# Kernel tuning notes

Measured on AMD Instinct MI355X. Metric: run time of the kernel, lower is better.

## Reference

```python
import jax, jax.numpy as jnp
import numpy as np

B, N, D, E = 4, 4096, 1024, 64
EPS = 1e-9
THRESH = 0.2            # second_threshold_eval
CAP_FACTOR = 2.0        # capacity_factor_eval
MIN_EXPERT_CAPACITY = 4


def setup_inputs() -> dict:
    key = jax.random.key(0)
    k1, k2 = jax.random.split(key)
    x = jax.random.normal(k1, (B, N, D), dtype=jnp.float32)
    w_gating = jax.random.normal(k2, (D, E), dtype=jnp.float32)
    return {"x": x, "w_gating": w_gating}


def _cumsum_exclusive(t, axis):
    # exclusive cumsum along `axis` (equivalent to pad-then-cumsum-then-slice)
    return jnp.cumsum(t, axis=axis) - t


def _gating(x, w_gating):
    b, n, d = x.shape
    e = w_gating.shape[-1]
    dt = x.dtype

    gate_logits = jnp.einsum('bnd,de->bne', x, w_gating)   # [b,n,e]
    raw_gates = jax.nn.softmax(gate_logits, axis=-1)

    index_1 = jnp.argmax(raw_gates, axis=-1)               # [b,n]
    gate_1 = jnp.max(raw_gates, axis=-1)                   # [b,n]
    mask_1 = jax.nn.one_hot(index_1, e, dtype=dt)          # [b,n,e]
    density_1_proxy = raw_gates

    gates_without_top_1 = raw_gates * (1.0 - mask_1)
    index_2 = jnp.argmax(gates_without_top_1, axis=-1)
    gate_2 = jnp.max(gates_without_top_1, axis=-1)
    mask_2 = jax.nn.one_hot(index_2, e, dtype=dt)

    denom = gate_1 + gate_2 + EPS
    gate_1 = gate_1 / denom
    gate_2 = gate_2 / denom

    # load-balancing aux loss
    density_1 = jnp.mean(mask_1, axis=-2)                  # [b,e]
    density_proxy = jnp.mean(density_1_proxy, axis=-2)     # [b,e]
    loss = jnp.mean(density_proxy * density_1) * float(e * e)

    # second-expert policy: 'threshold'
    mask_2 = mask_2 * (gate_2 > THRESH).astype(dt)[..., None]

    expert_capacity = max(min(n, int(n * CAP_FACTOR / e)), MIN_EXPERT_CAPACITY)
    cap_f = float(expert_capacity)

    # capacity routing for top-1
    position_in_expert_1 = _cumsum_exclusive(mask_1, axis=-2) * mask_1
    mask_1 = mask_1 * (position_in_expert_1 < cap_f).astype(dt)
    mask_1_count = jnp.sum(mask_1, axis=-2, keepdims=True)  # [b,1,e]
    mask_1_flat = jnp.sum(mask_1, axis=-1)                  # [b,n]
    position_in_expert_1 = jnp.sum(position_in_expert_1, axis=-1)  # [b,n]
    gate_1 = gate_1 * mask_1_flat

    # capacity routing for top-2 (offset by top-1 counts)
    position_in_expert_2 = (_cumsum_exclusive(mask_2, axis=-2) + mask_1_count) * mask_2
    mask_2 = mask_2 * (position_in_expert_2 < cap_f).astype(dt)
    mask_2_flat = jnp.sum(mask_2, axis=-1)
    position_in_expert_2 = jnp.sum(position_in_expert_2, axis=-1)
    gate_2 = gate_2 * mask_2_flat

    # one_hot with out-of-range index -> all zeros, matching safe_one_hot's clipping
    oh_e1 = jax.nn.one_hot(index_1, e, dtype=dt)
    oh_e2 = jax.nn.one_hot(index_2, e, dtype=dt)
    oh_c1 = jax.nn.one_hot(position_in_expert_1.astype(jnp.int32), expert_capacity, dtype=dt)
    oh_c2 = jax.nn.one_hot(position_in_expert_2.astype(jnp.int32), expert_capacity, dtype=dt)

    combine_tensor = (
        (gate_1 * mask_1_flat)[..., None, None] * oh_e1[..., :, None] * oh_c1[..., None, :]
        + (gate_2 * mask_2_flat)[..., None, None] * oh_e2[..., :, None] * oh_c2[..., None, :]
    )  # [b,n,e,capacity]

    router_z_loss = jnp.mean(jnp.sum(jax.nn.logsumexp(gate_logits, axis=-1), axis=-1))
    return combine_tensor, loss, router_z_loss


def reference(x, w_gating):
    combine_tensor, loss, router_z_loss = _gating(x, w_gating)
    dispatch_tensor = (combine_tensor != 0).astype(combine_tensor.dtype)
    return dispatch_tensor, combine_tensor, loss, router_z_loss
```

## Files before the change

kernel.cpp:

```cpp
#include <hip/hip_runtime.h>


#define B_DIM 4
#define N_DIM 4096
#define D_DIM 1024
#define E_DIM 64
#define CAP   128
#define NTOK  (B_DIM * N_DIM)
#define TM    32
#define TK    64
#define GATE_BLOCKS 512
#define ZERO_BLOCKS 8192

#define WS_IDX1  0
#define WS_IDX2  65536
#define WS_G1    131072
#define WS_G2    196608
#define WS_DENS  262144
#define WS_ZSUM  263168

__global__ __launch_bounds__(256) void fused_gating_zero(
    const float* __restrict__ x, const float* __restrict__ w,
    int* __restrict__ idx1, int* __restrict__ idx2,
    float* __restrict__ g1o, float* __restrict__ g2o,
    float* __restrict__ dens, float* __restrict__ zsum,
    float* __restrict__ out, size_t half) {
  __shared__ __align__(16) char smem[(TM * 68 + TK * E_DIM) * 4];
  const int t = threadIdx.x;

  if (blockIdx.x >= GATE_BLOCKS) {
    const int zb = blockIdx.x - GATE_BLOCKS;
    float4* o4 = (float4*)out;
    const size_t base = (size_t)zb * (256 * 32) + t;
    const float4 z = make_float4(0.f, 0.f, 0.f, 0.f);
#pragma unroll
    for (int i = 0; i < 32; ++i) o4[base + (size_t)i * 256] = z;
    if (zb == 0 && t == 0) { out[2 * half] = 0.f; out[2 * half + 1] = 0.f; }
    return;
  }

  float (*As)[68]   = (float(*)[68])smem;
  float (*Bs)[E_DIM] = (float(*)[E_DIM])(smem + TM * 68 * 4);
  double (*Ld)[65]  = (double(*)[65])smem;

  const int tokBase = blockIdx.x * TM;
  const int e4 = t & 15;
  const int tokg = t >> 4;
  const int tok0 = 2 * tokg, e0 = 4 * e4;

  double acc[2][4] = {};

  for (int k0 = 0; k0 < D_DIM; k0 += TK) {
    {
      const int d4 = t & 15, row = t >> 4;
      float4 va = *(const float4*)(x + (size_t)(tokBase + row) * D_DIM + k0 + 4 * d4);
      float4 vb = *(const float4*)(x + (size_t)(tokBase + row + 16) * D_DIM + k0 + 4 * d4);
      *(float4*)&As[row][4 * d4] = va;
      *(float4*)&As[row + 16][4 * d4] = vb;
    }
    {
      const float4* wsrc = (const float4*)(w + (size_t)k0 * E_DIM);
      float4* bdst = (float4*)&Bs[0][0];
      bdst[t]       = wsrc[t];
      bdst[t + 256] = wsrc[t + 256];
      bdst[t + 512] = wsrc[t + 512];
      bdst[t + 768] = wsrc[t + 768];
    }
    __syncthreads();
#pragma unroll 8
    for (int kk = 0; kk < TK; ++kk) {
      float a0 = As[tok0][kk], a1 = As[tok0 + 1][kk];
      float4 bv = *(float4*)&Bs[kk][e0];
      double da0 = (double)a0, da1 = (double)a1;
      double b0 = (double)bv.x, b1 = (double)bv.y, b2 = (double)bv.z, b3 = (double)bv.w;
      acc[0][0] += da0 * b0; acc[0][1] += da0 * b1; acc[0][2] += da0 * b2; acc[0][3] += da0 * b3;
      acc[1][0] += da1 * b0; acc[1][1] += da1 * b1; acc[1][2] += da1 * b2; acc[1][3] += da1 * b3;
    }
    __syncthreads();
  }

#pragma unroll
  for (int i = 0; i < 2; ++i)
#pragma unroll
    for (int j = 0; j < 4; ++j) Ld[tok0 + i][e0 + j] = acc[i][j];
  __syncthreads();

  const int wave = t >> 6;
  const int lane = t & 63;
  const int b = tokBase >> 12;
  float densacc = 0.f, zacc = 0.f;

  for (int s = 0; s < 8; ++s) {
    const int tok = wave * 8 + s;
    const double l = Ld[tok][lane];

    double mv = l; int mi = lane;
#pragma unroll
    for (int off = 32; off; off >>= 1) {
      double ov = __shfl_xor(mv, off);
      int oi = __shfl_xor(mi, off);
      if (ov > mv || (ov == mv && oi < mi)) { mv = ov; mi = oi; }
    }
    float p = expf((float)(l - mv));
    float sum = p;
#pragma unroll
    for (int off = 32; off; off >>= 1) sum += __shfl_xor(sum, off);

    double l2 = (lane == mi) ? -1.0e300 : l;
    double mv2 = l2; int mi2 = lane;
#pragma unroll
    for (int off = 32; off; off >>= 1) {
      double ov = __shfl_xor(mv2, off);
      int oi = __shfl_xor(mi2, off);
      if (ov > mv2 || (ov == mv2 && oi < mi2)) { mv2 = ov; mi2 = oi; }
    }

    float gate1 = 1.0f / sum;
    float gate2 = expf((float)(mv2 - mv)) / sum;
    float denom = gate1 + gate2 + 1e-9f;
    float g1n = gate1 / denom, g2n = gate2 / denom;
    int i2eff = (g2n > 0.2f) ? mi2 : -1;
    float lse = (float)mv + logf(sum);

    densacc += p;
    if (lane == 0) {
      const int gt = tokBase + tok;
      idx1[gt] = mi; idx2[gt] = i2eff;
      g1o[gt] = g1n; g2o[gt] = g2n;
      zacc += lse;
    }
  }
  atomicAdd(&dens[(b << 6) + lane], densacc);
  if (lane == 0) atomicAdd(zsum, zacc);
}

__global__ __launch_bounds__(256) void scan_scatter(
    const int* __restrict__ idx1, const int* __restrict__ idx2,
    const float* __restrict__ g1, const float* __restrict__ g2,
    const float* __restrict__ dens, const float* __restrict__ zsum,
    float* __restrict__ out, size_t half) {
  const int bid = blockIdx.x;
  const int b = bid >> 6, e = bid & 63;
  const int wv = threadIdx.x >> 6, lane = threadIdx.x & 63;
  const int tokBase = b * N_DIM + wv * 1024;
  const unsigned long long lmask = (1ull << lane) - 1ull;
  __shared__ int wcnt[4];

  float* dispatch = out;
  float* combine = out + half;
  unsigned long long bal[16];

  int c = 0;
#pragma unroll
  for (int ch = 0; ch < 16; ++ch) {
    bool m = (idx1[tokBase + ch * 64 + lane] == e);
    bal[ch] = __ballot(m);
    c += __popcll(bal[ch]);
  }
  if (lane == 0) wcnt[wv] = c;
  __syncthreads();
  int pre = 0, tot = 0;
#pragma unroll
  for (int wvi = 0; wvi < 4; ++wvi) {
    int v = wcnt[wvi];
    if (wvi < wv) pre += v;
    tot += v;
  }
  int run = pre;
#pragma unroll
  for (int ch = 0; ch < 16; ++ch) {
    unsigned long long bb = bal[ch];
    if ((bb >> lane) & 1ull) {
      int p = run + __popcll(bb & lmask);
      if (p < CAP) {
        int tok = tokBase + ch * 64 + lane;
        size_t off = ((size_t)tok * E_DIM + e) * CAP + p;
        dispatch[off] = 1.0f;
        combine[off] = g1[tok];
      }
    }
    run += __popcll(bb);
  }
  __syncthreads();

  const int off0 = tot < CAP ? tot : CAP;
  int c2 = 0;
#pragma unroll
  for (int ch = 0; ch < 16; ++ch) {
    bool m = (idx2[tokBase + ch * 64 + lane] == e);
    bal[ch] = __ballot(m);
    c2 += __popcll(bal[ch]);
  }
  if (lane == 0) wcnt[wv] = c2;
  __syncthreads();
  int pre2 = 0;
#pragma unroll
  for (int wvi = 0; wvi < 4; ++wvi)
    if (wvi < wv) pre2 += wcnt[wvi];
  int run2 = off0 + pre2;
#pragma unroll
  for (int ch = 0; ch < 16; ++ch) {
    unsigned long long bb = bal[ch];
    if ((bb >> lane) & 1ull) {
      int p = run2 + __popcll(bb & lmask);
      if (p < CAP) {
        int tok = tokBase + ch * 64 + lane;
        size_t off = ((size_t)tok * E_DIM + e) * CAP + p;
        dispatch[off] = 1.0f;
        combine[off] = g2[tok];
      }
    }
    run2 += __popcll(bb);
  }

  if (threadIdx.x == 0) {
    atomicAdd(&out[2 * half], dens[bid] * (float)tot * (1.0f / 1048576.0f));
    if (bid == 0) out[2 * half + 1] = zsum[0] * 0.25f;
  }
}

extern "C" void kernel_launch(void* const* d_in, const int* in_sizes, int n_in,
                              void* d_out, int out_size, void* d_ws, size_t ws_size,
                              hipStream_t stream) {
  const float* x = (const float*)d_in[0];
  const float* w = (const float*)d_in[1];
  float* out = (float*)d_out;
  char* ws = (char*)d_ws;

  int*   idx1 = (int*)(ws + WS_IDX1);
  int*   idx2 = (int*)(ws + WS_IDX2);
  float* g1   = (float*)(ws + WS_G1);
  float* g2   = (float*)(ws + WS_G2);
  float* dens = (float*)(ws + WS_DENS);
  float* zsum = (float*)(ws + WS_ZSUM);

  const size_t half = ((size_t)out_size - 2) / 2;

  hipMemsetAsync(ws + WS_DENS, 0, 257 * sizeof(float), stream);

  fused_gating_zero<<<GATE_BLOCKS + ZERO_BLOCKS, 256, 0, stream>>>(
      x, w, idx1, idx2, g1, g2, dens, zsum, out, half);

  scan_scatter<<<B_DIM * E_DIM, 256, 0, stream>>>(idx1, idx2, g1, g2,
                                                  dens, zsum, out, half);
}
```

Measured before the change: 1.111 ms.

## Write combine tensor densely in scan kernel and zero only dispatch half

The zeroing pass now clears only the dispatch half of the output. The scan kernel builds a per-token position and value table in shared memory and writes every row of the combine tensor, zeros included, with coalesced float4 stores, so combine is no longer zeroed and then scattered. The gating GEMM tile grows to 64 tokens with 4x4 double accumulators per thread, and the density and z-loss reductions now use per-block partial sums instead of global atomics and a memset. The density proxy is also corrected to use normalised softmax probabilities. The risk is that combine is now written by only 256 blocks, which may not saturate memory bandwidth.

New measurement: 1.180 ms. 6.2% more time.

```diff
diff --git a/kernel.cpp b/kernel.cpp
--- a/kernel.cpp
+++ b/kernel.cpp
@@ -6,32 +6,32 @@
 #define D_DIM 1024
 #define E_DIM 64
 #define CAP   128
-#define NTOK  (B_DIM * N_DIM)
-#define TM    32
+#define NTOK  16384
+#define TM    64
 #define TK    64
-#define GATE_BLOCKS 512
-#define ZERO_BLOCKS 8192
+#define GATE_BLOCKS 256
+#define ZERO_BLOCKS 4096
 
 #define WS_IDX1  0
 #define WS_IDX2  65536
 #define WS_G1    131072
 #define WS_G2    196608
 #define WS_DENS  262144
-#define WS_ZSUM  263168
+#define WS_Z     327680
 
 __global__ __launch_bounds__(256) void fused_gating_zero(
     const float* __restrict__ x, const float* __restrict__ w,
     int* __restrict__ idx1, int* __restrict__ idx2,
     float* __restrict__ g1o, float* __restrict__ g2o,
-    float* __restrict__ dens, float* __restrict__ zsum,
+    float* __restrict__ densPart, float* __restrict__ zPart,
     float* __restrict__ out, size_t half) {
-  __shared__ __align__(16) char smem[(TM * 68 + TK * E_DIM) * 4];
+  __shared__ __align__(16) char smem[33792];
   const int t = threadIdx.x;
 
   if (blockIdx.x >= GATE_BLOCKS) {
     const int zb = blockIdx.x - GATE_BLOCKS;
     float4* o4 = (float4*)out;
-    const size_t base = (size_t)zb * (256 * 32) + t;
+    const size_t base = (size_t)zb * 8192 + t;
     const float4 z = make_float4(0.f, 0.f, 0.f, 0.f);
 #pragma unroll
     for (int i = 0; i < 32; ++i) o4[base + (size_t)i * 256] = z;
@@ -39,59 +39,54 @@
     return;
   }
 
-  float (*As)[68]   = (float(*)[68])smem;
-  float (*Bs)[E_DIM] = (float(*)[E_DIM])(smem + TM * 68 * 4);
-  double (*Ld)[65]  = (double(*)[65])smem;
+  float (*As)[68] = (float(*)[68])smem;
+  float (*Bs)[64] = (float(*)[64])(smem + 17408);
+  double (*Ld)[65] = (double(*)[65])smem;
 
   const int tokBase = blockIdx.x * TM;
-  const int e4 = t & 15;
-  const int tokg = t >> 4;
-  const int tok0 = 2 * tokg, e0 = 4 * e4;
-
-  double acc[2][4] = {};
+  const int tok0 = 4 * (t >> 4), e0 = 4 * (t & 15);
+
+  double acc[4][4] = {};
 
   for (int k0 = 0; k0 < D_DIM; k0 += TK) {
     {
-      const int d4 = t & 15, row = t >> 4;
-      float4 va = *(const float4*)(x + (size_t)(tokBase + row) * D_DIM + k0 + 4 * d4);
-      float4 vb = *(const float4*)(x + (size_t)(tokBase + row + 16) * D_DIM + k0 + 4 * d4);
-      *(float4*)&As[row][4 * d4] = va;
-      *(float4*)&As[row + 16][4 * d4] = vb;
-    }
-    {
+      const int d4 = t & 15, rowb = t >> 4;
+#pragma unroll
+      for (int r = 0; r < 4; ++r) {
+        float4 v = *(const float4*)(x + (size_t)(tokBase + rowb + 16 * r) * D_DIM + k0 + 4 * d4);
+        *(float4*)&As[rowb + 16 * r][4 * d4] = v;
+      }
       const float4* wsrc = (const float4*)(w + (size_t)k0 * E_DIM);
       float4* bdst = (float4*)&Bs[0][0];
-      bdst[t]       = wsrc[t];
-      bdst[t + 256] = wsrc[t + 256];
-      bdst[t + 512] = wsrc[t + 512];
-      bdst[t + 768] = wsrc[t + 768];
+#pragma unroll
+      for (int i = 0; i < 4; ++i) bdst[t + 256 * i] = wsrc[t + 256 * i];
     }
     __syncthreads();
-#pragma unroll 8
+#pragma unroll 4
     for (int kk = 0; kk < TK; ++kk) {
-      float a0 = As[tok0][kk], a1 = As[tok0 + 1][kk];
       float4 bv = *(float4*)&Bs[kk][e0];
-      double da0 = (double)a0, da1 = (double)a1;
-      double b0 = (double)bv.x, b1 = (double)bv.y, b2 = (double)bv.z, b3 = (double)bv.w;
-      acc[0][0] += da0 * b0; acc[0][1] += da0 * b1; acc[0][2] += da0 * b2; acc[0][3] += da0 * b3;
-      acc[1][0] += da1 * b0; acc[1][1] += da1 * b1; acc[1][2] += da1 * b2; acc[1][3] += da1 * b3;
+      double b0 = bv.x, b1 = bv.y, b2 = bv.z, b3 = bv.w;
+      double a0 = As[tok0][kk], a1 = As[tok0 + 1][kk];
+      double a2 = As[tok0 + 2][kk], a3 = As[tok0 + 3][kk];
+      acc[0][0] += a0 * b0; acc[0][1] += a0 * b1; acc[0][2] += a0 * b2; acc[0][3] += a0 * b3;
+      acc[1][0] += a1 * b0; acc[1][1] += a1 * b1; acc[1][2] += a1 * b2; acc[1][3] += a1 * b3;
+      acc[2][0] += a2 * b0; acc[2][1] += a2 * b1; acc[2][2] += a2 * b2; acc[2][3] += a2 * b3;
+      acc[3][0] += a3 * b0; acc[3][1] += a3 * b1; acc[3][2] += a3 * b2; acc[3][3] += a3 * b3;
     }
     __syncthreads();
   }
 
 #pragma unroll
-  for (int i = 0; i < 2; ++i)
+  for (int i = 0; i < 4; ++i)
 #pragma unroll
     for (int j = 0; j < 4; ++j) Ld[tok0 + i][e0 + j] = acc[i][j];
   __syncthreads();
 
-  const int wave = t >> 6;
-  const int lane = t & 63;
-  const int b = tokBase >> 12;
+  const int wv = t >> 6, lane = t & 63;
   float densacc = 0.f, zacc = 0.f;
 
-  for (int s = 0; s < 8; ++s) {
-    const int tok = wave * 8 + s;
+  for (int s = 0; s < 16; ++s) {
+    const int tok = wv * 16 + s;
     const double l = Ld[tok][lane];
 
     double mv = l; int mi = lane;
@@ -122,7 +117,7 @@
     int i2eff = (g2n > 0.2f) ? mi2 : -1;
     float lse = (float)mv + logf(sum);
 
-    densacc += p;
+    densacc += p / sum;
     if (lane == 0) {
       const int gt = tokBase + tok;
       idx1[gt] = mi; idx2[gt] = i2eff;
@@ -130,24 +125,39 @@
       zacc += lse;
     }
   }
-  atomicAdd(&dens[(b << 6) + lane], densacc);
-  if (lane == 0) atomicAdd(zsum, zacc);
+
+  __syncthreads();
+  float* Ldns = (float*)smem;
+  float* Lz = (float*)(smem + 1024);
+  Ldns[wv * 64 + lane] = densacc;
+  if (lane == 0) Lz[wv] = zacc;
+  __syncthreads();
+  if (wv == 0) {
+    float d = Ldns[lane] + Ldns[64 + lane] + Ldns[128 + lane] + Ldns[192 + lane];
+    densPart[(blockIdx.x << 6) + lane] = d;
+    if (lane == 0) zPart[blockIdx.x] = Lz[0] + Lz[1] + Lz[2] + Lz[3];
+  }
 }
 
-__global__ __launch_bounds__(256) void scan_scatter(
+__global__ __launch_bounds__(256) void scan_write(
     const int* __restrict__ idx1, const int* __restrict__ idx2,
     const float* __restrict__ g1, const float* __restrict__ g2,
-    const float* __restrict__ dens, const float* __restrict__ zsum,
+    const float* __restrict__ densPart, const float* __restrict__ zPart,
     float* __restrict__ out, size_t half) {
-  const int bid = blockIdx.x;
-  const int b = bid >> 6, e = bid & 63;
+  __shared__ unsigned char posv[N_DIM];
+  __shared__ float valv[N_DIM];
+  __shared__ int wcnt[4];
+
+  const int bid = blockIdx.x, b = bid >> 6, e = bid & 63;
   const int wv = threadIdx.x >> 6, lane = threadIdx.x & 63;
   const int tokBase = b * N_DIM + wv * 1024;
   const unsigned long long lmask = (1ull << lane) - 1ull;
-  __shared__ int wcnt[4];
 
   float* dispatch = out;
-  float* combine = out + half;
+
+  ((int4*)posv)[threadIdx.x] = make_int4(-1, -1, -1, -1);
+  __syncthreads();
+
   unsigned long long bal[16];
 
   int c = 0;
@@ -173,10 +183,11 @@
     if ((bb >> lane) & 1ull) {
       int p = run + __popcll(bb & lmask);
       if (p < CAP) {
-        int tok = tokBase + ch * 64 + lane;
-        size_t off = ((size_t)tok * E_DIM + e) * CAP + p;
-        dispatch[off] = 1.0f;
-        combine[off] = g1[tok];
+        int gt = tokBase + ch * 64 + lane;
+        int tl = gt - b * N_DIM;
+        posv[tl] = (unsigned char)p;
+        valv[tl] = g1[gt];
+        dispatch[((size_t)gt * E_DIM + e) * CAP + p] = 1.0f;
       }
     }
     run += __popcll(bb);
@@ -204,18 +215,39 @@
     if ((bb >> lane) & 1ull) {
       int p = run2 + __popcll(bb & lmask);
       if (p < CAP) {
-        int tok = tokBase + ch * 64 + lane;
-        size_t off = ((size_t)tok * E_DIM + e) * CAP + p;
-        dispatch[off] = 1.0f;
-        combine[off] = g2[tok];
+        int gt = tokBase + ch * 64 + lane;
+        int tl = gt - b * N_DIM;
+        posv[tl] = (unsigned char)p;
+        valv[tl] = g2[gt];
+        dispatch[((size_t)gt * E_DIM + e) * CAP + p] = 1.0f;
       }
     }
     run2 += __popcll(bb);
   }
 
-  if (threadIdx.x == 0) {
-    atomicAdd(&out[2 * half], dens[bid] * (float)tot * (1.0f / 1048576.0f));
-    if (bid == 0) out[2 * half + 1] = zsum[0] * 0.25f;
+  if (wv == 0) {
+    float v = densPart[(((b << 6) + lane) << 6) + e];
+#pragma unroll
+    for (int off = 32; off; off >>= 1) v += __shfl_xor(v, off);
+    if (lane == 0)
+      atomicAdd(&out[2 * half], v * (float)tot * (1.0f / 1048576.0f));
+  }
+  if (bid == 0 && wv == 1) {
+    float v = zPart[lane] + zPart[lane + 64] + zPart[lane + 128] + zPart[lane + 192];
+#pragma unroll
+    for (int off = 32; off; off >>= 1) v += __shfl_xor(v, off);
+    if (lane == 0) out[2 * half + 1] = v * 0.25f;
+  }
+  __syncthreads();
+
+  const int grp = threadIdx.x >> 5, l = threadIdx.x & 31;
+  float4* comb4 = (float4*)(out + half);
+  for (int it = 0; it < 512; ++it) {
+    const int tl = it * 8 + grp;
+    const int pos = posv[tl];
+    float4 v = make_float4(0.f, 0.f, 0.f, 0.f);
+    if ((pos >> 2) == l) ((float*)&v)[pos & 3] = valv[tl];
+    comb4[((size_t)(b * N_DIM + tl) * E_DIM + e) * 32 + l] = v;
   }
 }
 
@@ -231,16 +263,14 @@
   int*   idx2 = (int*)(ws + WS_IDX2);
   float* g1   = (float*)(ws + WS_G1);
   float* g2   = (float*)(ws + WS_G2);
-  float* dens = (float*)(ws + WS_DENS);
-  float* zsum = (float*)(ws + WS_ZSUM);
+  float* densPart = (float*)(ws + WS_DENS);
+  float* zPart    = (float*)(ws + WS_Z);
 
   const size_t half = ((size_t)out_size - 2) / 2;
 
-  hipMemsetAsync(ws + WS_DENS, 0, 257 * sizeof(float), stream);
-
   fused_gating_zero<<<GATE_BLOCKS + ZERO_BLOCKS, 256, 0, stream>>>(
-      x, w, idx1, idx2, g1, g2, dens, zsum, out, half);
-
-  scan_scatter<<<B_DIM * E_DIM, 256, 0, stream>>>(idx1, idx2, g1, g2,
-                                                  dens, zsum, out, half);
+      x, w, idx1, idx2, g1, g2, densPart, zPart, out, half);
+
+  scan_write<<<B_DIM * E_DIM, 256, 0, stream>>>(idx1, idx2, g1, g2,
+                                                densPart, zPart, out, half);
 }
```
